# Kernel optimization log

Measured on AMD Instinct MI355X. Metric: run time of the kernel, lower is better.

The kernel has to match this reference:

```python
import jax, jax.numpy as jnp
import numpy as np

H = 64  # lstm hidden size
SLOPE = 0.01  # LeakyReLU default negative slope


def _leaky(x):
    return jnp.where(x >= 0, x, SLOPE * x)


def setup_inputs() -> dict:
    key = jax.random.key(0)
    ks = jax.random.split(key, 20)
    B, T = 32768, 200
    s = 0.1
    inp = {
        "noise": jax.random.normal(ks[0], (B, 3), jnp.float32),
        "w_ih0": jax.random.normal(ks[1], (4 * H, 3), jnp.float32) * s,
        "w_hh0": jax.random.normal(ks[2], (4 * H, H), jnp.float32) * s,
        "b_ih0": jax.random.normal(ks[3], (4 * H,), jnp.float32) * s,
        "b_hh0": jax.random.normal(ks[4], (4 * H,), jnp.float32) * s,
        "w_ih1": jax.random.normal(ks[5], (4 * H, H), jnp.float32) * s,
        "w_hh1": jax.random.normal(ks[6], (4 * H, H), jnp.float32) * s,
        "b_ih1": jax.random.normal(ks[7], (4 * H,), jnp.float32) * s,
        "b_hh1": jax.random.normal(ks[8], (4 * H,), jnp.float32) * s,
        "w_ih2": jax.random.normal(ks[9], (4 * H, H), jnp.float32) * s,
        "w_hh2": jax.random.normal(ks[10], (4 * H, H), jnp.float32) * s,
        "b_ih2": jax.random.normal(ks[11], (4 * H,), jnp.float32) * s,
        "b_hh2": jax.random.normal(ks[12], (4 * H,), jnp.float32) * s,
        "w1": jax.random.normal(ks[13], (32, H), jnp.float32) * s,
        "b1": jax.random.normal(ks[14], (32,), jnp.float32) * s,
        "w2": jax.random.normal(ks[15], (16, 32), jnp.float32) * s,
        "b2": jax.random.normal(ks[16], (16,), jnp.float32) * s,
        "w3": jax.random.normal(ks[17], (3, 16), jnp.float32) * s,
        "b3": jax.random.normal(ks[18], (3,), jnp.float32) * s,
        "length": T,
    }
    return inp


def _forward(noise, w_ih0, w_hh0, b_ih0, b_hh0, w_ih1, w_hh1, b_ih1, b_hh1,
             w_ih2, w_hh2, b_ih2, b_hh2, w1, b1, w2, b2, w3, b3, length):
    B = noise.shape[0]
    layers = [(w_ih0, w_hh0, b_ih0, b_hh0),
              (w_ih1, w_hh1, b_ih1, b_hh1),
              (w_ih2, w_hh2, b_ih2, b_hh2)]

    def cell(x, h, c, wih, whh, bih, bhh):
        # PyTorch LSTM gate order: i, f, g, o
        g = x @ wih.T + h @ whh.T + (bih + bhh)
        i, f, gg, o = jnp.split(g, 4, axis=-1)
        c_new = jax.nn.sigmoid(f) * c + jax.nn.sigmoid(i) * jnp.tanh(gg)
        h_new = jax.nn.sigmoid(o) * jnp.tanh(c_new)
        return h_new, c_new

    def step(carry, _):
        x, hs, cs = carry  # x: (B,3), hs/cs: (3,B,H)
        inp = x
        new_h, new_c = [], []
        for l, (wih, whh, bih, bhh) in enumerate(layers):
            h, c = cell(inp, hs[l], cs[l], wih, whh, bih, bhh)
            new_h.append(h)
            new_c.append(c)
            inp = h
        # MLP head (Dropout is identity in eval; LeakyReLU slope 0.01)
        y = _leaky(inp @ w1.T + b1)
        y = _leaky(y @ w2.T + b2)
        y = _leaky(y @ w3.T + b3)  # (B, 3)
        return (y, jnp.stack(new_h), jnp.stack(new_c)), y

    hs0 = jnp.zeros((3, B, H), noise.dtype)
    cs0 = jnp.zeros((3, B, H), noise.dtype)
    (_, _, _), ys = jax.lax.scan(step, (noise, hs0, cs0), None, length=length)
    return jnp.transpose(ys, (1, 0, 2))  # (B, T, 3)


def reference(noise, w_ih0, w_hh0, b_ih0, b_hh0, w_ih1, w_hh1, b_ih1, b_hh1,
              w_ih2, w_hh2, b_ih2, b_hh2, w1, b1, w2, b2, w3, b3, length):
    return _forward(noise, w_ih0, w_hh0, b_ih0, b_hh0, w_ih1, w_hh1, b_ih1,
                    b_hh1, w_ih2, w_hh2, b_ih2, b_hh2, w1, b1, w2, b2, w3,
                    b3, length)
```

## Files before the change

kernel.cpp:

```cpp
#include <hip/hip_runtime.h>

typedef __attribute__((ext_vector_type(4))) float  f32x4;
typedef __attribute__((ext_vector_type(8))) short  bf16x8;
typedef __attribute__((ext_vector_type(4))) short  bf16x4;

#define NTHR 1024
#define BT   128
#define L2E  1.4426950408889634f

#define PLANE(L)   ((L)*16384)
#define QB0        49152
#define QB1        65536
#define XFB_OFF    81920
#define Y1_OFF     83968
#define Y2_OFF     93184
#define BGL_OFF    97792
#define W0L_OFF    100864
#define B3L_OFF    104960
#define W3L_OFF    104976
#define OUT_OFF    105168
#define LDS_TOTAL  111312

__device__ __align__(16) unsigned char g_wsbuf[163840];

__device__ __forceinline__ unsigned short f2bf(float v) {
    unsigned int x = __float_as_uint(v);
    unsigned int r = x + 0x7fffu + ((x >> 16) & 1u);
    return (unsigned short)(r >> 16);
}
__device__ __forceinline__ float bf2f_lo(unsigned int d) { return __uint_as_float(d << 16); }
__device__ __forceinline__ float bf2f_hi(unsigned int d) { return __uint_as_float(d & 0xffff0000u); }

__device__ __forceinline__ float fsig2(float y) {
    return __builtin_amdgcn_rcpf(1.0f + __builtin_amdgcn_exp2f(-y));
}
__device__ __forceinline__ float ftanh2(float y) {
    return 1.0f - 2.0f * __builtin_amdgcn_rcpf(1.0f + __builtin_amdgcn_exp2f(y));
}
__device__ __forceinline__ float ftanhc(float c) {
    return 1.0f - 2.0f * __builtin_amdgcn_rcpf(1.0f + __builtin_amdgcn_exp2f(c * (2.0f * L2E)));
}

__global__ void prep_weights(const float* __restrict__ whh0, const float* __restrict__ wih1,
                             const float* __restrict__ whh1, const float* __restrict__ wih2,
                             const float* __restrict__ whh2)
{
    int gi = blockIdx.x * 256 + threadIdx.x;
    if (gi < 10240) {
        int m = gi / 2048;
        int rem = gi & 2047;
        int b = rem >> 6, l = rem & 63;
        int ks = b & 1, g = (b >> 1) & 3, ug = b >> 3;
        int row = g * 64 + ug * 16 + (l & 15);
        int kb  = ks * 32 + (l >> 4) * 8;
        float fac = (g == 2) ? (2.0f * L2E) : L2E;
        const float* src = (m == 0) ? whh0 : (m == 1) ? wih1 : (m == 2) ? whh1
                         : (m == 3) ? wih2 : whh2;
        unsigned short o[8];
        #pragma unroll
        for (int i = 0; i < 8; ++i)
            o[i] = f2bf(src[row * 64 + kb + i] * fac);
        unsigned char* dst = g_wsbuf + m * 32768 + b * 1024 + l * 16;
        #pragma unroll
        for (int i = 0; i < 8; ++i) ((unsigned short*)dst)[i] = o[i];
    }
}

#define MFMA_(A,B,C) __builtin_amdgcn_mfma_f32_16x16x32_bf16(A, B, C, 0, 0, 0)

#define BARX do { \
    asm volatile("s_waitcnt lgkmcnt(0)" ::: "memory"); \
    __builtin_amdgcn_s_barrier(); \
    __builtin_amdgcn_sched_barrier(0); \
    } while (0)

#define LOADQ(m, ks, R) \
    R = *(const bf16x8*)(g_wsbuf + (m) * 32768 + \
        ((tid >> 6) * 2 + (ks)) * 1024 + (tid & 63) * 16)
#define COMMITQ(R, BUF) \
    *(bf16x8*)(lds + (BUF) + tid * 16) = R

#define ACC_INIT(L) do { \
    _Pragma("unroll") for (int g_ = 0; g_ < 4; ++g_) { \
        float b_ = *(const float*)(lds + BGL_OFF + ((L) * 256 + g_ * 64 + u) * 4); \
        f32x4 t_ = {b_, b_, b_, b_}; \
        acc[g_][0] = t_; acc[g_][1] = t_; \
    } } while (0)

#define GATEP(APL, ks, BUF) do { \
    bf16x8 b_[4]; \
    _Pragma("unroll") for (int g_ = 0; g_ < 4; ++g_) \
        b_[g_] = *(const bf16x8*)(lds + (BUF) + (ug * 4 + g_) * 1024 + lane * 16); \
    _Pragma("unroll") for (int mt_ = 0; mt_ < 2; ++mt_) { \
        int ab_ = (((mbase + mt_ * 16 + l15) * 128 + (ks) * 64 + l4 * 16)) ^ rswz; \
        bf16x8 ah_ = *(const bf16x8*)(lds + PLANE(APL) + ab_); \
        _Pragma("unroll") for (int g_ = 0; g_ < 4; ++g_) \
            acc[g_][mt_] = MFMA_(ah_, b_[g_], acc[g_][mt_]); \
    } } while (0)

#define CELLW(L, CARR) do { \
    _Pragma("unroll") for (int mt_ = 0; mt_ < 2; ++mt_) \
    _Pragma("unroll") for (int r_ = 0; r_ < 4; ++r_) { \
        float gi_ = fsig2(acc[0][mt_][r_]); \
        float gf_ = fsig2(acc[1][mt_][r_]); \
        float gg_ = ftanh2(acc[2][mt_][r_]); \
        float go_ = fsig2(acc[3][mt_][r_]); \
        float cn_ = gf_ * CARR[mt_ * 4 + r_] + gi_ * gg_; \
        CARR[mt_ * 4 + r_] = cn_; \
        float hn_ = go_ * ftanhc(cn_); \
        int e_ = mbase + mt_ * 16 + l4 * 4 + r_; \
        int wb_ = ((e_ * 128 + u * 2)) ^ ((e_ & 7) << 4); \
        *(unsigned short*)(lds + PLANE(L) + wb_) = f2bf(hn_); \
    } } while (0)

#define XPART do { \
    _Pragma("unroll") for (int mt_ = 0; mt_ < 2; ++mt_) \
    _Pragma("unroll") for (int r_ = 0; r_ < 4; ++r_) { \
        int e_ = mbase + mt_ * 16 + l4 * 4 + r_; \
        f32x4 xv_ = *(const f32x4*)(lds + XFB_OFF + e_ * 16); \
        _Pragma("unroll") for (int g_ = 0; g_ < 4; ++g_) { \
            f32x4 w0_ = *(const f32x4*)(lds + W0L_OFF + (g_ * 64 + u) * 16); \
            acc[g_][mt_][r_] += xv_.x * w0_.x + xv_.y * w0_.y + xv_.z * w0_.z; \
        } } } while (0)

#define MLP1 do { \
    int Mt_ = wv >> 1; \
    f32x4 a1_ = {b1r, b1r, b1r, b1r}; \
    { int ab_ = (((Mt_ * 16 + l15) * 128 + 0 * 64 + l4 * 16)) ^ rswz; \
      bf16x8 ah_ = *(const bf16x8*)(lds + PLANE(2) + ab_); \
      a1_ = MFMA_(ah_, w1f0, a1_); } \
    { int ab_ = (((Mt_ * 16 + l15) * 128 + 1 * 64 + l4 * 16)) ^ rswz; \
      bf16x8 ah_ = *(const bf16x8*)(lds + PLANE(2) + ab_); \
      a1_ = MFMA_(ah_, w1f1, a1_); } \
    _Pragma("unroll") for (int r_ = 0; r_ < 4; ++r_) { \
        float y_ = a1_[r_]; y_ = (y_ >= 0.f) ? y_ : 0.01f * y_; \
        int e_ = Mt_ * 16 + l4 * 4 + r_; \
        *(unsigned short*)(lds + Y1_OFF + e_ * 72 + hf * 32 + l15 * 2) = f2bf(y_); \
    } } while (0)

#define MLP2M do { \
    if (wv < 8) { \
        bf16x4 alo_ = *(const bf16x4*)(lds + Y1_OFF + (wv * 16 + l15) * 72 + l4 * 16); \
        bf16x4 ahi_ = *(const bf16x4*)(lds + Y1_OFF + (wv * 16 + l15) * 72 + l4 * 16 + 8); \
        bf16x8 af_ = {alo_[0], alo_[1], alo_[2], alo_[3], \
                      ahi_[0], ahi_[1], ahi_[2], ahi_[3]}; \
        f32x4 a2_ = {b2r, b2r, b2r, b2r}; \
        a2_ = MFMA_(af_, w2f, a2_); \
        _Pragma("unroll") for (int r_ = 0; r_ < 4; ++r_) { \
            float y_ = a2_[r_]; y_ = (y_ >= 0.f) ? y_ : 0.01f * y_; \
            int e_ = wv * 16 + l4 * 4 + r_; \
            *(unsigned short*)(lds + Y2_OFF + e_ * 36 + l15 * 2) = f2bf(y_); \
        } } } while (0)

#define MLP3_OUT do { \
    if (tid < 384) { \
        int e3_ = tid & 127, r3_ = tid >> 7; \
        float a3_ = *(const float*)(lds + B3L_OFF + r3_ * 4); \
        _Pragma("unroll") for (int kd_ = 0; kd_ < 8; ++kd_) { \
            unsigned int d_ = *(const unsigned int*)(lds + Y2_OFF + e3_ * 36 + kd_ * 4); \
            a3_ = fmaf(bf2f_lo(d_), *(const float*)(lds + W3L_OFF + (r3_ * 16 + kd_ * 2) * 4),     a3_); \
            a3_ = fmaf(bf2f_hi(d_), *(const float*)(lds + W3L_OFF + (r3_ * 16 + kd_ * 2 + 1) * 4), a3_); \
        } \
        float y_ = (a3_ >= 0.f) ? a3_ : 0.01f * a3_; \
        *(float*)(lds + XFB_OFF + e3_ * 16 + r3_ * 4) = y_; \
        *(float*)(lds + OUT_OFF + e3_ * 48 + (t & 3) * 12 + r3_ * 4) = y_; \
    } } while (0)

extern "C" __global__ void __launch_bounds__(NTHR)
__attribute__((amdgpu_waves_per_eu(4, 4)))
lstm_mfma(const float* __restrict__ noise,
          const float* __restrict__ wih0, const float* __restrict__ whh0,
          const float* __restrict__ bih0, const float* __restrict__ bhh0,
          const float* __restrict__ wih1, const float* __restrict__ whh1,
          const float* __restrict__ bih1, const float* __restrict__ bhh1,
          const float* __restrict__ wih2, const float* __restrict__ whh2,
          const float* __restrict__ bih2, const float* __restrict__ bhh2,
          const float* __restrict__ w1g, const float* __restrict__ b1g,
          const float* __restrict__ w2g, const float* __restrict__ b2g,
          const float* __restrict__ w3g, const float* __restrict__ b3g,
          const int* __restrict__ lenp, float* __restrict__ out)
{
    extern __shared__ unsigned char lds[];
    const int tid  = threadIdx.x;
    const int lane = tid & 63;
    const int wv   = tid >> 6;
    const int ug   = wv & 3;
    const int mh   = wv >> 2;
    const int l15  = lane & 15;
    const int l4   = lane >> 4;
    const int u    = ug * 16 + l15;
    const int mbase = mh * 32;
    const int rswz  = (lane & 7) << 4;
    const int hf    = wv & 1;
    const int T = *lenp;
    const long eg0  = (long)blockIdx.x * BT;
    const long outs = 3L * T;

    float c0[8], c1[8], c2[8];
    #pragma unroll
    for (int i = 0; i < 8; ++i) { c0[i] = 0.f; c1[i] = 0.f; c2[i] = 0.f; }

    bf16x8 w1f0, w1f1, w2f;
    {
        const float* p0 = w1g + (hf * 16 + l15) * 64 + l4 * 8;
        w1f0 = (bf16x8){(short)f2bf(p0[0]), (short)f2bf(p0[1]), (short)f2bf(p0[2]),
                        (short)f2bf(p0[3]), (short)f2bf(p0[4]), (short)f2bf(p0[5]),
                        (short)f2bf(p0[6]), (short)f2bf(p0[7])};
        const float* p1 = p0 + 32;
        w1f1 = (bf16x8){(short)f2bf(p1[0]), (short)f2bf(p1[1]), (short)f2bf(p1[2]),
                        (short)f2bf(p1[3]), (short)f2bf(p1[4]), (short)f2bf(p1[5]),
                        (short)f2bf(p1[6]), (short)f2bf(p1[7])};
        const float* p2 = w2g + l15 * 32 + l4 * 8;
        w2f  = (bf16x8){(short)f2bf(p2[0]), (short)f2bf(p2[1]), (short)f2bf(p2[2]),
                        (short)f2bf(p2[3]), (short)f2bf(p2[4]), (short)f2bf(p2[5]),
                        (short)f2bf(p2[6]), (short)f2bf(p2[7])};
    }
    const float b1r = b1g[hf * 16 + l15];
    const float b2r = b2g[l15];

    bf16x8 RB, RC, RT;
    LOADQ(1, 0, RT);
    LOADQ(1, 1, RB);
    LOADQ(2, 0, RC);

    for (int i = tid; i < 49152 / 4; i += NTHR) ((unsigned int*)lds)[i] = 0u;
    if (tid < BT) {
        const float* np = noise + (eg0 + tid) * 3;
        f32x4 xv = {np[0], np[1], np[2], 0.f};
        *(f32x4*)(lds + XFB_OFF + tid * 16) = xv;
    }
    if (tid < 768) {
        int l = tid >> 8, r = tid & 255, g = r >> 6;
        float fac = (g == 2) ? (2.0f * L2E) : L2E;
        const float* bi = (l == 0) ? bih0 : ((l == 1) ? bih1 : bih2);
        const float* bh = (l == 0) ? bhh0 : ((l == 1) ? bhh1 : bhh2);
        *(float*)(lds + BGL_OFF + tid * 4) = (bi[r] + bh[r]) * fac;
    }
    if (tid < 256) {
        int g = tid >> 6;
        float fac = (g == 2) ? (2.0f * L2E) : L2E;
        f32x4 wv0 = {wih0[tid * 3] * fac, wih0[tid * 3 + 1] * fac,
                     wih0[tid * 3 + 2] * fac, 0.f};
        *(f32x4*)(lds + W0L_OFF + tid * 16) = wv0;
    }
    if (tid < 3)  *(float*)(lds + B3L_OFF + tid * 4) = b3g[tid];
    if (tid < 48) *(float*)(lds + W3L_OFF + tid * 4) = w3g[tid];

    __syncthreads();
    COMMITQ(RT, QB0);

    f32x4 acc[4][2];
    ACC_INIT(0);
    __syncthreads();

    #pragma unroll 1
    for (int t = 0; t < T; ++t) {
        XPART;
        CELLW(0, c0);
        BARX;
        COMMITQ(RB, QB1); LOADQ(2, 1, RB);
        ACC_INIT(1);
        GATEP(0, 0, QB0);
        BARX;
        COMMITQ(RC, QB0); LOADQ(3, 0, RC);
        GATEP(0, 1, QB1);
        BARX;
        COMMITQ(RB, QB1); LOADQ(3, 1, RB);
        GATEP(1, 0, QB0);
        BARX;
        COMMITQ(RC, QB0); LOADQ(4, 0, RC);
        GATEP(1, 1, QB1);
        BARX;
        CELLW(1, c1);
        BARX;
        COMMITQ(RB, QB1); LOADQ(4, 1, RB);
        ACC_INIT(2);
        GATEP(1, 0, QB0);
        BARX;
        COMMITQ(RC, QB0); LOADQ(0, 0, RC);
        GATEP(1, 1, QB1);
        BARX;
        COMMITQ(RB, QB1); LOADQ(0, 1, RB);
        GATEP(2, 0, QB0);
        BARX;
        COMMITQ(RC, QB0); LOADQ(1, 0, RC);
        GATEP(2, 1, QB1);
        BARX;
        CELLW(2, c2);
        BARX;
        COMMITQ(RB, QB1); LOADQ(1, 1, RB);
        MLP1;
        ACC_INIT(0);
        GATEP(0, 0, QB0);
        BARX;
        COMMITQ(RC, QB0); LOADQ(2, 0, RC);
        MLP2M;
        GATEP(0, 1, QB1);
        BARX;
        MLP3_OUT;
        if ((t & 3) == 3) {
            BARX;
            long tb = t - 3;
            #pragma unroll
            for (int it = 0; it < 2; ++it) {
                int i = it * NTHR + tid;
                if (i < 1536) {
                    int e = i / 12, j = i - e * 12;
                    out[(eg0 + e) * outs + tb * 3 + j] =
                        *(const float*)(lds + OUT_OFF + e * 48 + j * 4);
                }
            }
        }
        BARX;
    }

    int nst = T & 3;
    if (nst) {
        int nfl = BT * nst * 3;
        for (int i = tid; i < nfl; i += NTHR) {
            int e = i / (nst * 3), j = i - e * (nst * 3);
            out[(eg0 + e) * outs + (long)(T - nst) * 3 + j] =
                *(const float*)(lds + OUT_OFF + e * 48 + j * 4);
        }
    }
}

extern "C" void kernel_launch(void* const* d_in, const int* in_sizes, int n_in,
                              void* d_out, int out_size, void* d_ws, size_t ws_size,
                              hipStream_t stream)
{
    const float* noise = (const float*)d_in[0];
    const float* wih0  = (const float*)d_in[1];
    const float* whh0  = (const float*)d_in[2];
    const float* bih0  = (const float*)d_in[3];
    const float* bhh0  = (const float*)d_in[4];
    const float* wih1  = (const float*)d_in[5];
    const float* whh1  = (const float*)d_in[6];
    const float* bih1  = (const float*)d_in[7];
    const float* bhh1  = (const float*)d_in[8];
    const float* wih2  = (const float*)d_in[9];
    const float* whh2  = (const float*)d_in[10];
    const float* bih2  = (const float*)d_in[11];
    const float* bhh2  = (const float*)d_in[12];
    const float* w1g   = (const float*)d_in[13];
    const float* b1g   = (const float*)d_in[14];
    const float* w2g   = (const float*)d_in[15];
    const float* b2g   = (const float*)d_in[16];
    const float* w3g   = (const float*)d_in[17];
    const float* b3g   = (const float*)d_in[18];
    const int*   lenp  = (const int*)d_in[19];
    float* out = (float*)d_out;

    int B = in_sizes[0] / 3;
    int grid = B / BT;

    prep_weights<<<40, 256, 0, stream>>>(whh0, wih1, whh1, wih2, whh2);

    hipFuncSetAttribute((const void*)lstm_mfma,
                        hipFuncAttributeMaxDynamicSharedMemorySize, LDS_TOTAL);
    lstm_mfma<<<grid, NTHR, LDS_TOTAL, stream>>>(
        noise, wih0, whh0, bih0, bhh0, wih1, whh1, bih1, bhh1,
        wih2, whh2, bih2, bhh2, w1g, b1g, w2g, b2g, w3g, b3g, lenp, out);
}
```

Measured before the change: 3.681 ms.

## Overlap LSTM layer gate matmuls with five-slot weight staging ring and dual accumulators

Restructures the per-timestep schedule. Weight slices are staged through a five-slot LDS ring instead of two buffers, and two accumulator sets let the next layer's gate MFMAs overlap the current layer's cell update. This cuts the number of barriers per step. MLP weights now live in LDS rather than registers, freeing VGPRs, and output flushing happens every 2 steps instead of 4. The cost is a much larger LDS footprint (about 162 KB) and more complex ordering, where an error in slot rotation would silently corrupt results.

Result: slower. 4.230 ms (+14.9%).

```diff
diff --git a/kernel.cpp b/kernel.cpp
--- a/kernel.cpp
+++ b/kernel.cpp
@@ -9,17 +9,18 @@
 #define L2E  1.4426950408889634f
 
 #define PLANE(L)   ((L)*16384)
-#define QB0        49152
-#define QB1        65536
-#define XFB_OFF    81920
-#define Y1_OFF     83968
-#define Y2_OFF     93184
-#define BGL_OFF    97792
-#define W0L_OFF    100864
-#define B3L_OFF    104960
-#define W3L_OFF    104976
-#define OUT_OFF    105168
-#define LDS_TOTAL  111312
+#define QS(s)      (49152 + (s)*16384)
+#define XFB_OFF    131072
+#define Y1_OFF     133120
+#define Y2_OFF     142336
+#define BGL_OFF    146944
+#define W0L_OFF    150016
+#define B3L_OFF    154112
+#define W3L_OFF    154128
+#define W1L_OFF    154320
+#define W2L_OFF    158416
+#define OUT_OFF    159440
+#define LDS_TOTAL  162512
 
 __device__ __align__(16) unsigned char g_wsbuf[163840];
 
@@ -80,14 +81,14 @@
 #define COMMITQ(R, BUF) \
     *(bf16x8*)(lds + (BUF) + tid * 16) = R
 
-#define ACC_INIT(L) do { \
+#define ACC_INIT(L, ACC) do { \
     _Pragma("unroll") for (int g_ = 0; g_ < 4; ++g_) { \
         float b_ = *(const float*)(lds + BGL_OFF + ((L) * 256 + g_ * 64 + u) * 4); \
         f32x4 t_ = {b_, b_, b_, b_}; \
-        acc[g_][0] = t_; acc[g_][1] = t_; \
-    } } while (0)
-
-#define GATEP(APL, ks, BUF) do { \
+        ACC[g_][0] = t_; ACC[g_][1] = t_; \
+    } } while (0)
+
+#define GATEP(ACC, APL, ks, BUF) do { \
     bf16x8 b_[4]; \
     _Pragma("unroll") for (int g_ = 0; g_ < 4; ++g_) \
         b_[g_] = *(const bf16x8*)(lds + (BUF) + (ug * 4 + g_) * 1024 + lane * 16); \
@@ -95,16 +96,16 @@
         int ab_ = (((mbase + mt_ * 16 + l15) * 128 + (ks) * 64 + l4 * 16)) ^ rswz; \
         bf16x8 ah_ = *(const bf16x8*)(lds + PLANE(APL) + ab_); \
         _Pragma("unroll") for (int g_ = 0; g_ < 4; ++g_) \
-            acc[g_][mt_] = MFMA_(ah_, b_[g_], acc[g_][mt_]); \
-    } } while (0)
-
-#define CELLW(L, CARR) do { \
+            ACC[g_][mt_] = MFMA_(ah_, b_[g_], ACC[g_][mt_]); \
+    } } while (0)
+
+#define CELLW(L, CARR, ACC) do { \
     _Pragma("unroll") for (int mt_ = 0; mt_ < 2; ++mt_) \
     _Pragma("unroll") for (int r_ = 0; r_ < 4; ++r_) { \
-        float gi_ = fsig2(acc[0][mt_][r_]); \
-        float gf_ = fsig2(acc[1][mt_][r_]); \
-        float gg_ = ftanh2(acc[2][mt_][r_]); \
-        float go_ = fsig2(acc[3][mt_][r_]); \
+        float gi_ = fsig2(ACC[0][mt_][r_]); \
+        float gf_ = fsig2(ACC[1][mt_][r_]); \
+        float gg_ = ftanh2(ACC[2][mt_][r_]); \
+        float go_ = fsig2(ACC[3][mt_][r_]); \
         float cn_ = gf_ * CARR[mt_ * 4 + r_] + gi_ * gg_; \
         CARR[mt_ * 4 + r_] = cn_; \
         float hn_ = go_ * ftanhc(cn_); \
@@ -113,25 +114,27 @@
         *(unsigned short*)(lds + PLANE(L) + wb_) = f2bf(hn_); \
     } } while (0)
 
-#define XPART do { \
+#define XPART(ACC) do { \
     _Pragma("unroll") for (int mt_ = 0; mt_ < 2; ++mt_) \
     _Pragma("unroll") for (int r_ = 0; r_ < 4; ++r_) { \
         int e_ = mbase + mt_ * 16 + l4 * 4 + r_; \
         f32x4 xv_ = *(const f32x4*)(lds + XFB_OFF + e_ * 16); \
         _Pragma("unroll") for (int g_ = 0; g_ < 4; ++g_) { \
             f32x4 w0_ = *(const f32x4*)(lds + W0L_OFF + (g_ * 64 + u) * 16); \
-            acc[g_][mt_][r_] += xv_.x * w0_.x + xv_.y * w0_.y + xv_.z * w0_.z; \
+            ACC[g_][mt_][r_] += xv_.x * w0_.x + xv_.y * w0_.y + xv_.z * w0_.z; \
         } } } while (0)
 
 #define MLP1 do { \
     int Mt_ = wv >> 1; \
     f32x4 a1_ = {b1r, b1r, b1r, b1r}; \
+    bf16x8 wh0_ = *(const bf16x8*)(lds + W1L_OFF + (hf * 2 + 0) * 1024 + lane * 16); \
+    bf16x8 wh1_ = *(const bf16x8*)(lds + W1L_OFF + (hf * 2 + 1) * 1024 + lane * 16); \
     { int ab_ = (((Mt_ * 16 + l15) * 128 + 0 * 64 + l4 * 16)) ^ rswz; \
       bf16x8 ah_ = *(const bf16x8*)(lds + PLANE(2) + ab_); \
-      a1_ = MFMA_(ah_, w1f0, a1_); } \
+      a1_ = MFMA_(ah_, wh0_, a1_); } \
     { int ab_ = (((Mt_ * 16 + l15) * 128 + 1 * 64 + l4 * 16)) ^ rswz; \
       bf16x8 ah_ = *(const bf16x8*)(lds + PLANE(2) + ab_); \
-      a1_ = MFMA_(ah_, w1f1, a1_); } \
+      a1_ = MFMA_(ah_, wh1_, a1_); } \
     _Pragma("unroll") for (int r_ = 0; r_ < 4; ++r_) { \
         float y_ = a1_[r_]; y_ = (y_ >= 0.f) ? y_ : 0.01f * y_; \
         int e_ = Mt_ * 16 + l4 * 4 + r_; \
@@ -144,15 +147,16 @@
         bf16x4 ahi_ = *(const bf16x4*)(lds + Y1_OFF + (wv * 16 + l15) * 72 + l4 * 16 + 8); \
         bf16x8 af_ = {alo_[0], alo_[1], alo_[2], alo_[3], \
                       ahi_[0], ahi_[1], ahi_[2], ahi_[3]}; \
+        bf16x8 w2f_ = *(const bf16x8*)(lds + W2L_OFF + (l15 * 32 + l4 * 8) * 2); \
         f32x4 a2_ = {b2r, b2r, b2r, b2r}; \
-        a2_ = MFMA_(af_, w2f, a2_); \
+        a2_ = MFMA_(af_, w2f_, a2_); \
         _Pragma("unroll") for (int r_ = 0; r_ < 4; ++r_) { \
             float y_ = a2_[r_]; y_ = (y_ >= 0.f) ? y_ : 0.01f * y_; \
             int e_ = wv * 16 + l4 * 4 + r_; \
             *(unsigned short*)(lds + Y2_OFF + e_ * 36 + l15 * 2) = f2bf(y_); \
         } } } while (0)
 
-#define MLP3_OUT do { \
+#define MLP3_OUT(tc) do { \
     if (tid < 384) { \
         int e3_ = tid & 127, r3_ = tid >> 7; \
         float a3_ = *(const float*)(lds + B3L_OFF + r3_ * 4); \
@@ -163,7 +167,7 @@
         } \
         float y_ = (a3_ >= 0.f) ? a3_ : 0.01f * a3_; \
         *(float*)(lds + XFB_OFF + e3_ * 16 + r3_ * 4) = y_; \
-        *(float*)(lds + OUT_OFF + e3_ * 48 + (t & 3) * 12 + r3_ * 4) = y_; \
+        *(float*)(lds + OUT_OFF + e3_ * 24 + ((tc) & 1) * 12 + r3_ * 4) = y_; \
     } } while (0)
 
 extern "C" __global__ void __launch_bounds__(NTHR)
@@ -200,28 +204,13 @@
     #pragma unroll
     for (int i = 0; i < 8; ++i) { c0[i] = 0.f; c1[i] = 0.f; c2[i] = 0.f; }
 
-    bf16x8 w1f0, w1f1, w2f;
-    {
-        const float* p0 = w1g + (hf * 16 + l15) * 64 + l4 * 8;
-        w1f0 = (bf16x8){(short)f2bf(p0[0]), (short)f2bf(p0[1]), (short)f2bf(p0[2]),
-                        (short)f2bf(p0[3]), (short)f2bf(p0[4]), (short)f2bf(p0[5]),
-                        (short)f2bf(p0[6]), (short)f2bf(p0[7])};
-        const float* p1 = p0 + 32;
-        w1f1 = (bf16x8){(short)f2bf(p1[0]), (short)f2bf(p1[1]), (short)f2bf(p1[2]),
-                        (short)f2bf(p1[3]), (short)f2bf(p1[4]), (short)f2bf(p1[5]),
-                        (short)f2bf(p1[6]), (short)f2bf(p1[7])};
-        const float* p2 = w2g + l15 * 32 + l4 * 8;
-        w2f  = (bf16x8){(short)f2bf(p2[0]), (short)f2bf(p2[1]), (short)f2bf(p2[2]),
-                        (short)f2bf(p2[3]), (short)f2bf(p2[4]), (short)f2bf(p2[5]),
-                        (short)f2bf(p2[6]), (short)f2bf(p2[7])};
-    }
     const float b1r = b1g[hf * 16 + l15];
     const float b2r = b2g[l15];
 
-    bf16x8 RB, RC, RT;
-    LOADQ(1, 0, RT);
-    LOADQ(1, 1, RB);
-    LOADQ(2, 0, RC);
+    bf16x8 Ra, Rb;
+
+    LOADQ(2, 0, Ra);
+    LOADQ(2, 1, Rb);
 
     for (int i = tid; i < 49152 / 4; i += NTHR) ((unsigned int*)lds)[i] = 0u;
     if (tid < BT) {
@@ -243,84 +232,91 @@
                      wih0[tid * 3 + 2] * fac, 0.f};
         *(f32x4*)(lds + W0L_OFF + tid * 16) = wv0;
     }
-    if (tid < 3)  *(float*)(lds + B3L_OFF + tid * 4) = b3g[tid];
-    if (tid < 48) *(float*)(lds + W3L_OFF + tid * 4) = w3g[tid];
+    if (tid < 256) {
+        int b = tid >> 6, l = tid & 63;
+        int hh = b >> 1, ks = b & 1;
+        int row = hh * 16 + (l & 15);
+        int kb  = ks * 32 + (l >> 4) * 8;
+        unsigned short o[8];
+        #pragma unroll
+        for (int i = 0; i < 8; ++i) o[i] = f2bf(w1g[row * 64 + kb + i]);
+        #pragma unroll
+        for (int i = 0; i < 8; ++i)
+            *(unsigned short*)(lds + W1L_OFF + b * 1024 + l * 16 + i * 2) = o[i];
+    }
+    if (tid < 512) *(unsigned short*)(lds + W2L_OFF + tid * 2) = f2bf(w2g[tid]);
+    if (tid < 3)   *(float*)(lds + B3L_OFF + tid * 4) = b3g[tid];
+    if (tid < 48)  *(float*)(lds + W3L_OFF + tid * 4) = w3g[tid];
 
     __syncthreads();
-    COMMITQ(RT, QB0);
-
-    f32x4 acc[4][2];
-    ACC_INIT(0);
+    COMMITQ(Ra, QS(0));
+    COMMITQ(Rb, QS(1));
+    LOADQ(1, 0, Ra);
+    LOADQ(1, 1, Rb);
+    COMMITQ(Ra, QS(2));
+    COMMITQ(Rb, QS(3));
+    LOADQ(4, 0, Ra);
+
+    f32x4 accA[4][2], accB[4][2];
+    ACC_INIT(0, accA);
     __syncthreads();
 
     #pragma unroll 1
     for (int t = 0; t < T; ++t) {
-        XPART;
-        CELLW(0, c0);
-        BARX;
-        COMMITQ(RB, QB1); LOADQ(2, 1, RB);
-        ACC_INIT(1);
-        GATEP(0, 0, QB0);
-        BARX;
-        COMMITQ(RC, QB0); LOADQ(3, 0, RC);
-        GATEP(0, 1, QB1);
-        BARX;
-        COMMITQ(RB, QB1); LOADQ(3, 1, RB);
-        GATEP(1, 0, QB0);
-        BARX;
-        COMMITQ(RC, QB0); LOADQ(4, 0, RC);
-        GATEP(1, 1, QB1);
-        BARX;
-        CELLW(1, c1);
-        BARX;
-        COMMITQ(RB, QB1); LOADQ(4, 1, RB);
-        ACC_INIT(2);
-        GATEP(1, 0, QB0);
-        BARX;
-        COMMITQ(RC, QB0); LOADQ(0, 0, RC);
-        GATEP(1, 1, QB1);
-        BARX;
-        COMMITQ(RB, QB1); LOADQ(0, 1, RB);
-        GATEP(2, 0, QB0);
-        BARX;
-        COMMITQ(RC, QB0); LOADQ(1, 0, RC);
-        GATEP(2, 1, QB1);
-        BARX;
-        CELLW(2, c2);
-        BARX;
-        COMMITQ(RB, QB1); LOADQ(1, 1, RB);
+        COMMITQ(Ra, QS(4)); LOADQ(4, 1, Ra);
+        XPART(accA); CELLW(0, c0, accA);
+        ACC_INIT(1, accB); GATEP(accB, 1, 0, QS(0));
+        BARX;
+        COMMITQ(Ra, QS(0)); LOADQ(3, 0, Ra);
+        GATEP(accB, 1, 1, QS(1)); GATEP(accB, 0, 0, QS(2));
+        BARX;
+        COMMITQ(Ra, QS(1)); LOADQ(3, 1, Ra); LOADQ(0, 1, Rb);
+        GATEP(accB, 0, 1, QS(3));
+        ACC_INIT(2, accA); GATEP(accA, 2, 0, QS(4));
+        BARX;
+        COMMITQ(Ra, QS(2)); COMMITQ(Rb, QS(4)); LOADQ(0, 0, Ra);
+        CELLW(1, c1, accB);
+        GATEP(accA, 2, 1, QS(0));
+        BARX;
+        COMMITQ(Ra, QS(3)); LOADQ(2, 0, Ra);
+        GATEP(accA, 1, 0, QS(1)); GATEP(accA, 1, 1, QS(2));
+        BARX;
+        COMMITQ(Ra, QS(0)); LOADQ(2, 1, Ra);
+        CELLW(2, c2, accA);
+        ACC_INIT(0, accB); GATEP(accB, 0, 0, QS(3));
+        BARX;
+        COMMITQ(Ra, QS(1)); LOADQ(1, 0, Ra);
         MLP1;
-        ACC_INIT(0);
-        GATEP(0, 0, QB0);
-        BARX;
-        COMMITQ(RC, QB0); LOADQ(2, 0, RC);
+        GATEP(accB, 0, 1, QS(4));
+        BARX;
+        COMMITQ(Ra, QS(2)); LOADQ(1, 1, Ra);
         MLP2M;
-        GATEP(0, 1, QB1);
-        BARX;
-        MLP3_OUT;
-        if ((t & 3) == 3) {
+        BARX;
+        COMMITQ(Ra, QS(3)); LOADQ(4, 0, Ra);
+        MLP3_OUT(t);
+        if ((t & 1) == 1) {
             BARX;
-            long tb = t - 3;
-            #pragma unroll
-            for (int it = 0; it < 2; ++it) {
-                int i = it * NTHR + tid;
-                if (i < 1536) {
-                    int e = i / 12, j = i - e * 12;
-                    out[(eg0 + e) * outs + tb * 3 + j] =
-                        *(const float*)(lds + OUT_OFF + e * 48 + j * 4);
-                }
+            long tb = t - 1;
+            if (tid < 768) {
+                int e = tid / 6, rem = tid - e * 6;
+                int st = rem / 3, j = rem - st * 3;
+                out[(eg0 + e) * outs + (tb + st) * 3 + j] =
+                    *(const float*)(lds + OUT_OFF + e * 24 + st * 12 + j * 4);
             }
         }
         BARX;
-    }
-
-    int nst = T & 3;
-    if (nst) {
-        int nfl = BT * nst * 3;
-        for (int i = tid; i < nfl; i += NTHR) {
-            int e = i / (nst * 3), j = i - e * (nst * 3);
-            out[(eg0 + e) * outs + (long)(T - nst) * 3 + j] =
-                *(const float*)(lds + OUT_OFF + e * 48 + j * 4);
+        #pragma unroll
+        for (int g = 0; g < 4; ++g) {
+            accA[g][0] = accB[g][0];
+            accA[g][1] = accB[g][1];
+        }
+    }
+
+    if (T & 1) {
+        if (tid < 384) {
+            int e = tid & 127, j = tid >> 7;
+            out[(eg0 + e) * outs + (long)(T - 1) * 3 + j] =
+                *(const float*)(lds + OUT_OFF + e * 24 + ((T - 1) & 1) * 12 + j * 4);
         }
     }
 }
```
